# Performance work log

Measured on AMD Instinct MI355X. Metric: run time of the kernel, lower is better.

Reference implementation:

```python
import jax, jax.numpy as jnp
import numpy as np

ALPHA = 0.2  # LeakyReLU negative slope


def setup_inputs() -> dict:
    key = jax.random.key(0)
    k1, k2, k3, k4 = jax.random.split(key, 4)
    B, N, F_IN, F_OUT = 8, 2048, 512, 256
    h = jax.random.normal(k1, (B, N, F_IN), dtype=jnp.float32)
    # torch nn.Linear weights: [out, in]
    W = jax.random.normal(k2, (F_OUT, F_IN), dtype=jnp.float32) * (1.414 / np.sqrt(F_IN))
    a1 = jax.random.normal(k3, (1, F_OUT), dtype=jnp.float32) * (1.414 / np.sqrt(F_OUT))
    a2 = jax.random.normal(k4, (1, F_OUT), dtype=jnp.float32) * (1.414 / np.sqrt(F_OUT))
    return {"h": h, "W": W, "a1": a1, "a2": a2}


def reference(h, W, a1, a2):
    # Wh: [B, N, F_out]
    Wh = jnp.einsum('bnf,of->bno', h, W)
    # additive attention scores
    s1 = jnp.einsum('bno,o->bn', Wh, a1[0])  # [B, N]
    s2 = jnp.einsum('bno,o->bn', Wh, a2[0])  # [B, N]
    e = s1[:, :, None] + s2[:, None, :]       # [B, N, N]
    e = jnp.where(e > 0, e, ALPHA * e)         # LeakyReLU
    attention = jax.nn.softmax(e, axis=2)      # softmax over last dim
    # dropout p=0.0 -> identity
    h_prime = jnp.einsum('bnm,bmo->bno', attention, Wh)
    return jax.nn.elu(h_prime)  # concat=True path
```

## Files before the change

kernel.cpp:

```cpp
#include <hip/hip_runtime.h>

typedef __attribute__((ext_vector_type(8))) _Float16 half8;
typedef __attribute__((ext_vector_type(4))) _Float16 half4;
typedef __attribute__((ext_vector_type(4))) float f32x4;

#define ALPHA 0.2f

__device__ __forceinline__ void gload_lds16(const void* g, void* l) {
  __builtin_amdgcn_global_load_lds((const __attribute__((address_space(1))) unsigned int*)g,
                                   (__attribute__((address_space(3))) unsigned int*)l, 16, 0, 0);
}

__global__ __launch_bounds__(256) void k_convW(const float* __restrict__ W,
                                               _Float16* __restrict__ W16) {
  int idx4 = blockIdx.x * 256 + threadIdx.x;
  int n = idx4 >> 7;
  int q = idx4 & 127;
  float4 v = *reinterpret_cast<const float4*>(W + n * 512 + q * 4);
  half4 hv = {(_Float16)v.x, (_Float16)v.y, (_Float16)v.z, (_Float16)v.w};
  int kp = (q * 4) ^ ((n & 7) << 3);
  *reinterpret_cast<half4*>(W16 + n * 512 + kp) = hv;
}

__global__ __launch_bounds__(256) void k_uvec(const float* __restrict__ W,
                                              const float* __restrict__ a1,
                                              const float* __restrict__ a2,
                                              float* __restrict__ u1,
                                              float* __restrict__ u2) {
  __shared__ float r1[4], r2[4];
  int k = blockIdx.x, t = threadIdx.x;
  float wv = W[t * 512 + k];
  float x1 = wv * a1[t];
  float x2 = wv * a2[t];
#pragma unroll
  for (int off = 32; off >= 1; off >>= 1) {
    x1 += __shfl_xor(x1, off);
    x2 += __shfl_xor(x2, off);
  }
  if ((t & 63) == 0) { r1[t >> 6] = x1; r2[t >> 6] = x2; }
  __syncthreads();
  if (t == 0) {
    u1[k] = r1[0] + r1[1] + r1[2] + r1[3];
    u2[k] = r2[0] + r2[1] + r2[2] + r2[3];
  }
}

__global__ __launch_bounds__(256) void k_smax(const float* __restrict__ s2,
                                              float* __restrict__ smax) {
  __shared__ float red[4];
  int b = blockIdx.x, t = threadIdx.x;
  float m = -1e30f;
  for (int j = t; j < 2048; j += 256) m = fmaxf(m, s2[b * 2048 + j]);
#pragma unroll
  for (int off = 32; off >= 1; off >>= 1) m = fmaxf(m, __shfl_xor(m, off));
  if ((t & 63) == 0) red[t >> 6] = m;
  __syncthreads();
  if (t == 0) smax[b] = fmaxf(fmaxf(red[0], red[1]), fmaxf(red[2], red[3]));
}

__global__ __launch_bounds__(256) void k_gemm_wh(const float* __restrict__ h,
                                                 const _Float16* __restrict__ W16,
                                                 const float* __restrict__ u1,
                                                 const float* __restrict__ u2,
                                                 float* __restrict__ s1o,
                                                 float* __restrict__ s2o,
                                                 _Float16* __restrict__ WhT) {
  __shared__ _Float16 Ab[2][32 * 64];
  __shared__ _Float16 Bb[2][256 * 64];
  const int t = threadIdx.x, lane = t & 63, w = t >> 6;
  const int i0 = blockIdx.x * 32;
  const int b = i0 >> 11, n0 = i0 & 2047;
  const int ar = t >> 3, au = t & 7;
  const float* hrow = h + (size_t)(i0 + ar) * 512 + au * 8;

  f32x4 acc[2][4];
#pragma unroll
  for (int mi = 0; mi < 2; ++mi)
#pragma unroll
    for (int ni = 0; ni < 4; ++ni) acc[mi][ni] = (f32x4){0.f, 0.f, 0.f, 0.f};

  float4 aR0 = *reinterpret_cast<const float4*>(hrow);
  float4 aR1 = *reinterpret_cast<const float4*>(hrow + 4);
#pragma unroll
  for (int q = 0; q < 8; ++q) {
    int idx = (q * 4 + w) * 64 + lane;
    int nn = idx >> 3, uu = idx & 7;
    gload_lds16(W16 + nn * 512 + uu * 8, (char*)&Bb[0][0] + idx * 16);
  }
  float x1 = 0.f, x2 = 0.f;

  for (int kt = 0; kt < 8; ++kt) {
    const int cur = kt & 1;
    {
      half8 av;
      av[0] = (_Float16)aR0.x; av[1] = (_Float16)aR0.y;
      av[2] = (_Float16)aR0.z; av[3] = (_Float16)aR0.w;
      av[4] = (_Float16)aR1.x; av[5] = (_Float16)aR1.y;
      av[6] = (_Float16)aR1.z; av[7] = (_Float16)aR1.w;
      *reinterpret_cast<half8*>((char*)&Ab[cur][0] + ar * 128 + ((au * 16) ^ ((ar & 7) << 4))) = av;
      const float* up1 = u1 + kt * 64 + au * 8;
      const float* up2 = u2 + kt * 64 + au * 8;
      float4 u1a = *reinterpret_cast<const float4*>(up1);
      float4 u1b = *reinterpret_cast<const float4*>(up1 + 4);
      float4 u2a = *reinterpret_cast<const float4*>(up2);
      float4 u2b = *reinterpret_cast<const float4*>(up2 + 4);
      x1 += aR0.x * u1a.x + aR0.y * u1a.y + aR0.z * u1a.z + aR0.w * u1a.w
          + aR1.x * u1b.x + aR1.y * u1b.y + aR1.z * u1b.z + aR1.w * u1b.w;
      x2 += aR0.x * u2a.x + aR0.y * u2a.y + aR0.z * u2a.z + aR0.w * u2a.w
          + aR1.x * u2b.x + aR1.y * u2b.y + aR1.z * u2b.z + aR1.w * u2b.w;
    }
    __syncthreads();
    if (kt < 7) {
      const int k0 = (kt + 1) * 64;
      aR0 = *reinterpret_cast<const float4*>(hrow + k0);
      aR1 = *reinterpret_cast<const float4*>(hrow + k0 + 4);
#pragma unroll
      for (int q = 0; q < 8; ++q) {
        int idx = (q * 4 + w) * 64 + lane;
        int nn = idx >> 3, uu = idx & 7;
        gload_lds16(W16 + nn * 512 + k0 + uu * 8, (char*)&Bb[cur ^ 1][0] + idx * 16);
      }
    }
    const char* Ac = (const char*)&Ab[cur][0];
    const char* Bc = (const char*)&Bb[cur][0];
#pragma unroll
    for (int kk = 0; kk < 2; ++kk) {
      const int jb = (lane >> 4) * 16 + kk * 64;
      half8 afr[2];
#pragma unroll
      for (int mi = 0; mi < 2; ++mi) {
        int rr = (lane & 15) + 16 * mi;
        afr[mi] = *reinterpret_cast<const half8*>(Ac + rr * 128 + (jb ^ ((rr & 7) << 4)));
      }
#pragma unroll
      for (int ni = 0; ni < 4; ++ni) {
        int nn = 64 * w + 16 * ni + (lane & 15);
        half8 bfr = *reinterpret_cast<const half8*>(Bc + nn * 128 + (jb ^ ((nn & 7) << 4)));
#pragma unroll
        for (int mi = 0; mi < 2; ++mi)
          acc[mi][ni] = __builtin_amdgcn_mfma_f32_16x16x32_f16(afr[mi], bfr, acc[mi][ni], 0, 0, 0);
      }
    }
  }
  x1 += __shfl_xor(x1, 1); x1 += __shfl_xor(x1, 2); x1 += __shfl_xor(x1, 4);
  x2 += __shfl_xor(x2, 1); x2 += __shfl_xor(x2, 2); x2 += __shfl_xor(x2, 4);
  if (au == 0) { s1o[i0 + ar] = x1; s2o[i0 + ar] = x2; }
  _Float16* whtb = WhT + (size_t)b * 256 * 2048;
#pragma unroll
  for (int mi = 0; mi < 2; ++mi)
#pragma unroll
    for (int ni = 0; ni < 4; ++ni) {
      int c = 64 * w + 16 * ni + (lane & 15);
      int nb = n0 + 16 * mi + (lane >> 4) * 4;
      int np = nb ^ ((c & 7) << 3);
      f32x4 a = acc[mi][ni];
      half4 hv = {(_Float16)a[0], (_Float16)a[1], (_Float16)a[2], (_Float16)a[3]};
      *reinterpret_cast<half4*>(whtb + (size_t)c * 2048 + np) = hv;
    }
}

__global__ __launch_bounds__(256) void k_attn(const _Float16* __restrict__ WhT,
                                              const float* __restrict__ s1,
                                              const float* __restrict__ s2,
                                              const float* __restrict__ smax,
                                              float* __restrict__ out) {
  __shared__ _Float16 Bb[2][128 * 64];
  const int t = threadIdx.x, lane = t & 63, w = t >> 6;
  const int bid = blockIdx.x;
  const int b = bid & 7;
  const int r = bid >> 3;
  const int i0 = (r & 31) * 64;
  const int c0 = (r >> 5) * 128;
  const _Float16* whtb = WhT + ((size_t)b * 256 + c0) * 2048;
  const float* s2b = s2 + b * 2048;
  const int arow = lane & 15;
  const int grow = i0 + w * 16 + arow;
  float s1v = s1[b * 2048 + grow];
  float mrow = s1v + smax[b];
  mrow = fmaxf(mrow, ALPHA * mrow);
  float dsum = 0.f;
  f32x4 acc[8];
#pragma unroll
  for (int ni = 0; ni < 8; ++ni) acc[ni] = (f32x4){0.f, 0.f, 0.f, 0.f};

#pragma unroll
  for (int q = 0; q < 4; ++q) {
    int idx = (q * 4 + w) * 64 + lane;
    int cl = idx >> 3, uu = idx & 7;
    gload_lds16(whtb + (size_t)cl * 2048 + uu * 8, (char*)&Bb[0][0] + idx * 16);
  }

  for (int jt = 0; jt < 32; ++jt) {
    const int cur = jt & 1;
    __syncthreads();
    if (jt < 31) {
      const int j0n = (jt + 1) * 64;
#pragma unroll
      for (int q = 0; q < 4; ++q) {
        int idx = (q * 4 + w) * 64 + lane;
        int cl = idx >> 3, uu = idx & 7;
        gload_lds16(whtb + (size_t)cl * 2048 + j0n + uu * 8, (char*)&Bb[cur ^ 1][0] + idx * 16);
      }
    }
    const int j0 = jt * 64;
    const char* Bc = (const char*)&Bb[cur][0];
#pragma unroll
    for (int kk = 0; kk < 2; ++kk) {
      const int jl = (lane >> 4) * 8 + kk * 32;
      float4 sA = *reinterpret_cast<const float4*>(s2b + j0 + jl);
      float4 sB = *reinterpret_cast<const float4*>(s2b + j0 + jl + 4);
      half8 afr;
      float e, p;
      e = s1v + sA.x; e = fmaxf(e, ALPHA * e); p = __expf(e - mrow); afr[0] = (_Float16)p; dsum += p;
      e = s1v + sA.y; e = fmaxf(e, ALPHA * e); p = __expf(e - mrow); afr[1] = (_Float16)p; dsum += p;
      e = s1v + sA.z; e = fmaxf(e, ALPHA * e); p = __expf(e - mrow); afr[2] = (_Float16)p; dsum += p;
      e = s1v + sA.w; e = fmaxf(e, ALPHA * e); p = __expf(e - mrow); afr[3] = (_Float16)p; dsum += p;
      e = s1v + sB.x; e = fmaxf(e, ALPHA * e); p = __expf(e - mrow); afr[4] = (_Float16)p; dsum += p;
      e = s1v + sB.y; e = fmaxf(e, ALPHA * e); p = __expf(e - mrow); afr[5] = (_Float16)p; dsum += p;
      e = s1v + sB.z; e = fmaxf(e, ALPHA * e); p = __expf(e - mrow); afr[6] = (_Float16)p; dsum += p;
      e = s1v + sB.w; e = fmaxf(e, ALPHA * e); p = __expf(e - mrow); afr[7] = (_Float16)p; dsum += p;
      const int jb = jl * 2;
#pragma unroll
      for (int ni = 0; ni < 8; ++ni) {
        int cl = 16 * ni + arow;
        half8 bfr = *reinterpret_cast<const half8*>(Bc + cl * 128 + (jb ^ ((cl & 7) << 4)));
        acc[ni] = __builtin_amdgcn_mfma_f32_16x16x32_f16(afr, bfr, acc[ni], 0, 0, 0);
      }
    }
  }
  dsum += __shfl_xor(dsum, 16);
  dsum += __shfl_xor(dsum, 32);
  float inv[4];
#pragma unroll
  for (int reg = 0; reg < 4; ++reg) {
    float d = __shfl(dsum, (lane >> 4) * 4 + reg);
    inv[reg] = 1.f / d;
  }
  const size_t ob = ((size_t)b * 2048 + i0 + w * 16) * 256 + c0;
#pragma unroll
  for (int ni = 0; ni < 8; ++ni) {
    int c = 16 * ni + arow;
#pragma unroll
    for (int reg = 0; reg < 4; ++reg) {
      int rr = (lane >> 4) * 4 + reg;
      float v = acc[ni][reg] * inv[reg];
      v = v > 0.f ? v : (__expf(v) - 1.f);
      out[ob + (size_t)rr * 256 + c] = v;
    }
  }
}

extern "C" void kernel_launch(void* const* d_in, const int* in_sizes, int n_in,
                              void* d_out, int out_size, void* d_ws, size_t ws_size,
                              hipStream_t stream) {
  (void)in_sizes; (void)n_in; (void)out_size; (void)ws_size;
  const float* h = (const float*)d_in[0];
  const float* W = (const float*)d_in[1];
  const float* a1 = (const float*)d_in[2];
  const float* a2 = (const float*)d_in[3];
  float* out = (float*)d_out;
  char* ws = (char*)d_ws;
  _Float16* WhT = (_Float16*)(ws);
  _Float16* W16 = (_Float16*)(ws + 8388608);
  float* u1 = (float*)(ws + 8650752);
  float* u2 = (float*)(ws + 8652800);
  float* s1 = (float*)(ws + 8654848);
  float* s2 = (float*)(ws + 8720384);
  float* smax = (float*)(ws + 8785920);

  hipLaunchKernelGGL(k_convW, dim3(128), dim3(256), 0, stream, W, W16);
  hipLaunchKernelGGL(k_uvec, dim3(512), dim3(256), 0, stream, W, a1, a2, u1, u2);
  hipLaunchKernelGGL(k_gemm_wh, dim3(512), dim3(256), 0, stream, h, W16, u1, u2, s1, s2, WhT);
  hipLaunchKernelGGL(k_smax, dim3(8), dim3(256), 0, stream, s2, smax);
  hipLaunchKernelGGL(k_attn, dim3(512), dim3(256), 0, stream, WhT, s1, s2, smax, out);
}
```

Baseline: 75.57 us.

## Compute attention probabilities once per tile into LDS and share across column groups

The attention kernel now uses 512-thread blocks covering 32 rows by all 256 output columns. Each probability is computed once by a dedicated thread mapping and stored as fp16 in a double-buffered LDS tile, instead of every column-split block recomputing the exp terms. The exponent is rewritten to use exp2 with log2e pre-scaled s2 values written by k_smax. The row sum is taken with an MFMA against a ones vector. The trade-off is more LDS traffic and an extra LDS tile, but redundant transcendental work is removed.

Result: faster. 70.87 us (-6.2%).

```diff
diff --git a/kernel.cpp b/kernel.cpp
--- a/kernel.cpp
+++ b/kernel.cpp
@@ -3,12 +3,24 @@
 typedef __attribute__((ext_vector_type(8))) _Float16 half8;
 typedef __attribute__((ext_vector_type(4))) _Float16 half4;
 typedef __attribute__((ext_vector_type(4))) float f32x4;
+#if __has_builtin(__builtin_amdgcn_cvt_pkrtz)
+typedef __attribute__((ext_vector_type(2))) __fp16 fp16x2;
+#endif
 
 #define ALPHA 0.2f
+#define LOG2E 1.44269504f
 
 __device__ __forceinline__ void gload_lds16(const void* g, void* l) {
   __builtin_amdgcn_global_load_lds((const __attribute__((address_space(1))) unsigned int*)g,
                                    (__attribute__((address_space(3))) unsigned int*)l, 16, 0, 0);
+}
+
+__device__ __forceinline__ float fexp2(float x) {
+#if __has_builtin(__builtin_amdgcn_exp2f)
+  return __builtin_amdgcn_exp2f(x);
+#else
+  return __expf(x * 0.69314718f);
+#endif
 }
 
 __global__ __launch_bounds__(256) void k_convW(const float* __restrict__ W,
@@ -46,11 +58,16 @@
 }
 
 __global__ __launch_bounds__(256) void k_smax(const float* __restrict__ s2,
-                                              float* __restrict__ smax) {
+                                              float* __restrict__ smax,
+                                              float* __restrict__ s2L) {
   __shared__ float red[4];
   int b = blockIdx.x, t = threadIdx.x;
   float m = -1e30f;
-  for (int j = t; j < 2048; j += 256) m = fmaxf(m, s2[b * 2048 + j]);
+  for (int j = t; j < 2048; j += 256) {
+    float v = s2[b * 2048 + j];
+    s2L[b * 2048 + j] = LOG2E * v;
+    m = fmaxf(m, v);
+  }
 #pragma unroll
   for (int off = 32; off >= 1; off >>= 1) m = fmaxf(m, __shfl_xor(m, off));
   if ((t & 63) == 0) red[t >> 6] = m;
@@ -159,35 +176,63 @@
     }
 }
 
-__global__ __launch_bounds__(256) void k_attn(const _Float16* __restrict__ WhT,
+__global__ __launch_bounds__(512) void k_attn(const _Float16* __restrict__ WhT,
                                               const float* __restrict__ s1,
-                                              const float* __restrict__ s2,
+                                              const float* __restrict__ s2L,
                                               const float* __restrict__ smax,
                                               float* __restrict__ out) {
-  __shared__ _Float16 Bb[2][128 * 64];
+  __shared__ _Float16 Bb[2][256 * 64];
+  __shared__ _Float16 Pb[2][32 * 64];
+  __shared__ float d_lds[32];
   const int t = threadIdx.x, lane = t & 63, w = t >> 6;
+  const int rg = w >> 2, cg = w & 3;
   const int bid = blockIdx.x;
   const int b = bid & 7;
-  const int r = bid >> 3;
-  const int i0 = (r & 31) * 64;
-  const int c0 = (r >> 5) * 128;
-  const _Float16* whtb = WhT + ((size_t)b * 256 + c0) * 2048;
-  const float* s2b = s2 + b * 2048;
+  const int i0 = (bid >> 3) * 32;
+  const _Float16* whtb = WhT + (size_t)b * 256 * 2048;
+  const float* s2Lb = s2L + b * 2048;
   const int arow = lane & 15;
-  const int grow = i0 + w * 16 + arow;
-  float s1v = s1[b * 2048 + grow];
-  float mrow = s1v + smax[b];
-  mrow = fmaxf(mrow, ALPHA * mrow);
-  float dsum = 0.f;
-  f32x4 acc[8];
-#pragma unroll
-  for (int ni = 0; ni < 8; ++ni) acc[ni] = (f32x4){0.f, 0.f, 0.f, 0.f};
+  const float sm = smax[b];
+  const int pr = t >> 4, pj = t & 15;
+  const float s1p = s1[b * 2048 + i0 + pr];
+  const float e0p = s1p + sm;
+  const float mrowp = fmaxf(e0p, ALPHA * e0p);
+  const float C1 = LOG2E * (s1p - mrowp);
+  const float C2 = fmaf(ALPHA * LOG2E, s1p, -LOG2E * mrowp);
+  const int pwoff = pr * 128 + ((pj * 8) ^ ((pr & 7) << 4));
+  half8 onesb;
+  {
+    _Float16 ov = (arow == 0) ? (_Float16)1.0f : (_Float16)0.0f;
+#pragma unroll
+    for (int x = 0; x < 8; ++x) onesb[x] = ov;
+  }
+  f32x4 acc[4];
+#pragma unroll
+  for (int ni = 0; ni < 4; ++ni) acc[ni] = (f32x4){0.f, 0.f, 0.f, 0.f};
+  f32x4 accd = (f32x4){0.f, 0.f, 0.f, 0.f};
 
 #pragma unroll
   for (int q = 0; q < 4; ++q) {
-    int idx = (q * 4 + w) * 64 + lane;
+    int idx = q * 512 + t;
     int cl = idx >> 3, uu = idx & 7;
     gload_lds16(whtb + (size_t)cl * 2048 + uu * 8, (char*)&Bb[0][0] + idx * 16);
+  }
+  {
+    float4 sv = *reinterpret_cast<const float4*>(s2Lb + pj * 4);
+    float p0 = fexp2(fmaxf(C1 + sv.x, fmaf(ALPHA, sv.x, C2)));
+    float p1 = fexp2(fmaxf(C1 + sv.y, fmaf(ALPHA, sv.y, C2)));
+    float p2 = fexp2(fmaxf(C1 + sv.z, fmaf(ALPHA, sv.z, C2)));
+    float p3 = fexp2(fmaxf(C1 + sv.w, fmaf(ALPHA, sv.w, C2)));
+    half4 hv;
+#if __has_builtin(__builtin_amdgcn_cvt_pkrtz)
+    fp16x2 q0 = __builtin_amdgcn_cvt_pkrtz(p0, p1);
+    fp16x2 q1 = __builtin_amdgcn_cvt_pkrtz(p2, p3);
+    hv[0] = (_Float16)q0[0]; hv[1] = (_Float16)q0[1];
+    hv[2] = (_Float16)q1[0]; hv[3] = (_Float16)q1[1];
+#else
+    hv[0] = (_Float16)p0; hv[1] = (_Float16)p1; hv[2] = (_Float16)p2; hv[3] = (_Float16)p3;
+#endif
+    *reinterpret_cast<half4*>((char*)&Pb[0][0] + pwoff) = hv;
   }
 
   for (int jt = 0; jt < 32; ++jt) {
@@ -197,53 +242,58 @@
       const int j0n = (jt + 1) * 64;
 #pragma unroll
       for (int q = 0; q < 4; ++q) {
-        int idx = (q * 4 + w) * 64 + lane;
+        int idx = q * 512 + t;
         int cl = idx >> 3, uu = idx & 7;
         gload_lds16(whtb + (size_t)cl * 2048 + j0n + uu * 8, (char*)&Bb[cur ^ 1][0] + idx * 16);
       }
-    }
-    const int j0 = jt * 64;
+      float4 sv = *reinterpret_cast<const float4*>(s2Lb + j0n + pj * 4);
+      float p0 = fexp2(fmaxf(C1 + sv.x, fmaf(ALPHA, sv.x, C2)));
+      float p1 = fexp2(fmaxf(C1 + sv.y, fmaf(ALPHA, sv.y, C2)));
+      float p2 = fexp2(fmaxf(C1 + sv.z, fmaf(ALPHA, sv.z, C2)));
+      float p3 = fexp2(fmaxf(C1 + sv.w, fmaf(ALPHA, sv.w, C2)));
+      half4 hv;
+#if __has_builtin(__builtin_amdgcn_cvt_pkrtz)
+      fp16x2 q0 = __builtin_amdgcn_cvt_pkrtz(p0, p1);
+      fp16x2 q1 = __builtin_amdgcn_cvt_pkrtz(p2, p3);
+      hv[0] = (_Float16)q0[0]; hv[1] = (_Float16)q0[1];
+      hv[2] = (_Float16)q1[0]; hv[3] = (_Float16)q1[1];
+#else
+      hv[0] = (_Float16)p0; hv[1] = (_Float16)p1; hv[2] = (_Float16)p2; hv[3] = (_Float16)p3;
+#endif
+      *reinterpret_cast<half4*>((char*)&Pb[cur ^ 1][0] + pwoff) = hv;
+    }
     const char* Bc = (const char*)&Bb[cur][0];
+    const char* Pc = (const char*)&Pb[cur][0];
 #pragma unroll
     for (int kk = 0; kk < 2; ++kk) {
-      const int jl = (lane >> 4) * 8 + kk * 32;
-      float4 sA = *reinterpret_cast<const float4*>(s2b + j0 + jl);
-      float4 sB = *reinterpret_cast<const float4*>(s2b + j0 + jl + 4);
-      half8 afr;
-      float e, p;
-      e = s1v + sA.x; e = fmaxf(e, ALPHA * e); p = __expf(e - mrow); afr[0] = (_Float16)p; dsum += p;
-      e = s1v + sA.y; e = fmaxf(e, ALPHA * e); p = __expf(e - mrow); afr[1] = (_Float16)p; dsum += p;
-      e = s1v + sA.z; e = fmaxf(e, ALPHA * e); p = __expf(e - mrow); afr[2] = (_Float16)p; dsum += p;
-      e = s1v + sA.w; e = fmaxf(e, ALPHA * e); p = __expf(e - mrow); afr[3] = (_Float16)p; dsum += p;
-      e = s1v + sB.x; e = fmaxf(e, ALPHA * e); p = __expf(e - mrow); afr[4] = (_Float16)p; dsum += p;
-      e = s1v + sB.y; e = fmaxf(e, ALPHA * e); p = __expf(e - mrow); afr[5] = (_Float16)p; dsum += p;
-      e = s1v + sB.z; e = fmaxf(e, ALPHA * e); p = __expf(e - mrow); afr[6] = (_Float16)p; dsum += p;
-      e = s1v + sB.w; e = fmaxf(e, ALPHA * e); p = __expf(e - mrow); afr[7] = (_Float16)p; dsum += p;
-      const int jb = jl * 2;
-#pragma unroll
-      for (int ni = 0; ni < 8; ++ni) {
-        int cl = 16 * ni + arow;
+      const int jb = ((lane >> 4) * 8 + kk * 32) * 2;
+      const int ar32 = rg * 16 + arow;
+      half8 afr = *reinterpret_cast<const half8*>(Pc + ar32 * 128 + (jb ^ ((ar32 & 7) << 4)));
+      if (cg == 0)
+        accd = __builtin_amdgcn_mfma_f32_16x16x32_f16(afr, onesb, accd, 0, 0, 0);
+#pragma unroll
+      for (int ni = 0; ni < 4; ++ni) {
+        int cl = cg * 64 + 16 * ni + arow;
         half8 bfr = *reinterpret_cast<const half8*>(Bc + cl * 128 + (jb ^ ((cl & 7) << 4)));
         acc[ni] = __builtin_amdgcn_mfma_f32_16x16x32_f16(afr, bfr, acc[ni], 0, 0, 0);
       }
     }
   }
-  dsum += __shfl_xor(dsum, 16);
-  dsum += __shfl_xor(dsum, 32);
-  float inv[4];
+  if (cg == 0 && arow == 0) {
+#pragma unroll
+    for (int reg = 0; reg < 4; ++reg)
+      d_lds[rg * 16 + (lane >> 4) * 4 + reg] = accd[reg];
+  }
+  __syncthreads();
+  const size_t ob = ((size_t)b * 2048 + i0 + rg * 16) * 256 + cg * 64;
 #pragma unroll
   for (int reg = 0; reg < 4; ++reg) {
-    float d = __shfl(dsum, (lane >> 4) * 4 + reg);
-    inv[reg] = 1.f / d;
-  }
-  const size_t ob = ((size_t)b * 2048 + i0 + w * 16) * 256 + c0;
-#pragma unroll
-  for (int ni = 0; ni < 8; ++ni) {
-    int c = 16 * ni + arow;
-#pragma unroll
-    for (int reg = 0; reg < 4; ++reg) {
-      int rr = (lane >> 4) * 4 + reg;
-      float v = acc[ni][reg] * inv[reg];
+    int rr = (lane >> 4) * 4 + reg;
+    float inv = 1.0f / d_lds[rg * 16 + rr];
+#pragma unroll
+    for (int ni = 0; ni < 4; ++ni) {
+      int c = 16 * ni + arow;
+      float v = acc[ni][reg] * inv;
       v = v > 0.f ? v : (__expf(v) - 1.f);
       out[ob + (size_t)rr * 256 + c] = v;
     }
@@ -267,10 +317,11 @@
   float* s1 = (float*)(ws + 8654848);
   float* s2 = (float*)(ws + 8720384);
   float* smax = (float*)(ws + 8785920);
+  float* s2L = (float*)(ws + 8785952);
 
   hipLaunchKernelGGL(k_convW, dim3(128), dim3(256), 0, stream, W, W16);
   hipLaunchKernelGGL(k_uvec, dim3(512), dim3(256), 0, stream, W, a1, a2, u1, u2);
   hipLaunchKernelGGL(k_gemm_wh, dim3(512), dim3(256), 0, stream, h, W16, u1, u2, s1, s2, WhT);
-  hipLaunchKernelGGL(k_smax, dim3(8), dim3(256), 0, stream, s2, smax);
-  hipLaunchKernelGGL(k_attn, dim3(512), dim3(256), 0, stream, WhT, s1, s2, smax, out);
-}
+  hipLaunchKernelGGL(k_smax, dim3(8), dim3(256), 0, stream, s2, smax, s2L);
+  hipLaunchKernelGGL(k_attn, dim3(512), dim3(512), 0, stream, WhT, s1, s2L, smax, out);
+}
```
